# Kernel optimization log

Hardware: AMD Instinct MI355X
Metric: run time of the kernel (lower is better)

Reference implementation:

```python
import jax, jax.numpy as jnp
import numpy as np

B, S, E = 4, 2048, 1024
H, DK = 16, 64

def setup_inputs() -> dict:
    key = jax.random.key(0)
    ks = jax.random.split(key, 9)
    sc = 1.0 / np.sqrt(E)
    return {
        "q": jax.random.normal(ks[0], (B, S, E), jnp.float32),
        "Wq": jax.random.normal(ks[1], (E, H * DK), jnp.float32) * sc,
        "bq": jax.random.normal(ks[2], (H * DK,), jnp.float32) * 0.01,
        "Wk": jax.random.normal(ks[3], (E, H * DK), jnp.float32) * sc,
        "bk": jax.random.normal(ks[4], (H * DK,), jnp.float32) * 0.01,
        "Wv": jax.random.normal(ks[5], (E, H * DK), jnp.float32) * sc,
        "bv": jax.random.normal(ks[6], (H * DK,), jnp.float32) * 0.01,
        "Wo": jax.random.normal(ks[7], (H * DK, E), jnp.float32) * sc,
        "bo": jax.random.normal(ks[8], (E,), jnp.float32) * 0.01,
    }

def _split_heads(x):
    # (B, S, H*DK) -> (B, H, S, DK)
    return x.reshape(B, S, H, DK).transpose(0, 2, 1, 3)

def reference(q, Wq, bq, Wk, bk, Wv, bv, Wo, bo):
    # self-attention: k = v = q (torch module path when k=v=None)
    qh = _split_heads(q @ Wq + bq)
    kh = _split_heads(q @ Wk + bk)
    vh = _split_heads(q @ Wv + bv)
    scale = 1.0 / jnp.sqrt(jnp.asarray(DK, qh.dtype))
    scores = jnp.einsum("bhqd,bhkd->bhqk", qh, kh) * scale  # (B,H,S,S)
    attn = jax.nn.softmax(scores, axis=-1)
    ctx = jnp.einsum("bhqk,bhkd->bhqd", attn, vh)
    ctx = ctx.transpose(0, 2, 1, 3).reshape(B, S, H * DK)
    return ctx @ Wo + bo
```

## Files before the change

kernel.cpp:

```cpp
#include <hip/hip_runtime.h>
#include <hip/hip_bf16.h>
#include <math.h>


typedef _Float16 f16x8 __attribute__((ext_vector_type(8)));
typedef _Float16 f16x4 __attribute__((ext_vector_type(4)));
typedef _Float16 f16x2 __attribute__((ext_vector_type(2)));
typedef float    f32x4 __attribute__((ext_vector_type(4)));
typedef unsigned int u32x2 __attribute__((ext_vector_type(2)));
typedef unsigned int u32x4 __attribute__((ext_vector_type(4)));

#define MFMA16(a,b,c) __builtin_amdgcn_mfma_f32_16x16x32_f16(a,b,c,0,0,0)

__device__ __forceinline__ void async_cp16(const _Float16* g, _Float16* l) {
    __builtin_amdgcn_global_load_lds(
        (const __attribute__((address_space(1))) unsigned int*)g,
        (__attribute__((address_space(3))) unsigned int*)l,
        16, 0, 0);
}

__device__ __forceinline__ f16x2 pk(float a, float b) {
    return __builtin_bit_cast(f16x2, __builtin_amdgcn_cvt_pkrtz(a, b));
}

__global__ void __launch_bounds__(256) prep_weights(
    const float* __restrict__ Wq, const float* __restrict__ Wk,
    const float* __restrict__ Wv, const float* __restrict__ Wo,
    _Float16* __restrict__ wt)
{
    __shared__ float tile[32][33];
    int mat = blockIdx.y;
    const float* W = (mat==0)?Wq:(mat==1)?Wk:(mat==2)?Wv:Wo;
    _Float16* WT = wt + (size_t)mat*1048576;
    int t = blockIdx.x;
    int kb = (t & 31) * 32;
    int nb = (t >> 5) * 32;
    int tx = threadIdx.x & 31, ty = threadIdx.x >> 5;
    #pragma unroll
    for (int r = 0; r < 4; ++r) {
        int row = ty + r*8;
        tile[row][tx] = W[(size_t)(kb+row)*1024 + nb + tx];
    }
    __syncthreads();
    #pragma unroll
    for (int r = 0; r < 4; ++r) {
        int row = ty + r*8;
        WT[(size_t)(nb+row)*1024 + kb + tx] = (_Float16)tile[tx][row];
    }
}

__global__ void __launch_bounds__(256) cvt_x(
    const float* __restrict__ X, _Float16* __restrict__ Xh)
{
    int i = (blockIdx.x*256 + threadIdx.x)*4;
    f32x4 x = *(const f32x4*)&X[i];
    f16x4 h;
    #pragma unroll
    for (int k=0;k<4;k++) h[k] = (_Float16)x[k];
    *(f16x4*)&Xh[i] = h;
}

__device__ __forceinline__ void stage_tile(
    const _Float16* __restrict__ Ag, const _Float16* __restrict__ Bg, int kb,
    _Float16* sAb, _Float16* sBb, int wave, int lane)
{
    #pragma unroll
    for (int j = 0; j < 4; ++j) {
        int d   = j*512 + wave*64 + lane;
        int row = d >> 3;
        int sg  = (d & 7) ^ (row & 7);
        async_cp16(&Ag[(size_t)row*1024 + kb + sg*8], sAb + (j*512 + wave*64)*8);
    }
    #pragma unroll
    for (int j = 0; j < 2; ++j) {
        int d   = j*512 + wave*64 + lane;
        int row = d >> 3;
        int sg  = (d & 7) ^ (row & 7);
        async_cp16(&Bg[(size_t)row*1024 + kb + sg*8], sBb + (j*512 + wave*64)*8);
    }
}

#define GEMM_K_LOOP(EXTRA_STAGE_GUARD)                                         \
    stage_tile(Ag, Bg, 0,  pA0, pB0, wave, lane);                              \
    stage_tile(Ag, Bg, 64, pA1, pB1, wave, lane);                              \
    asm volatile("s_waitcnt vmcnt(6)" ::: "memory");                           \
    __builtin_amdgcn_s_barrier();                                              \
    __builtin_amdgcn_sched_barrier(0);                                         \
    for (int t = 0; t < 16; ++t) {                                             \
        if (t + 2 < 16) stage_tile(Ag, Bg, (t+2)*64, pA2, pB2, wave, lane);    \
        f16x8 af[4][2], bf[4][2];                                              \
        _Pragma("unroll")                                                      \
        for (int i = 0; i < 4; ++i) {                                          \
            _Pragma("unroll")                                                  \
            for (int ks = 0; ks < 2; ++ks) {                                   \
                af[i][ks] = *(const f16x8*)&pA0[(wr*64+i*16+cc)*64 +           \
                                                (((ks*4+q4)^(cc&7))*8)];       \
                bf[i][ks] = *(const f16x8*)&pB0[(wc*64+i*16+cc)*64 +           \
                                                (((ks*4+q4)^(cc&7))*8)];       \
            }                                                                  \
        }                                                                      \
        __builtin_amdgcn_s_setprio(1);                                         \
        _Pragma("unroll")                                                      \
        for (int ks = 0; ks < 2; ++ks)                                         \
            _Pragma("unroll")                                                  \
            for (int i = 0; i < 4; ++i)                                        \
                _Pragma("unroll")                                              \
                for (int j = 0; j < 4; ++j)                                    \
                    acc[i][j] = MFMA16(af[i][ks], bf[j][ks], acc[i][j]);       \
        __builtin_amdgcn_s_setprio(0);                                         \
        if (t < 14) asm volatile("s_waitcnt vmcnt(6)" ::: "memory");           \
        else        asm volatile("s_waitcnt vmcnt(0)" ::: "memory");           \
        __builtin_amdgcn_s_barrier();                                          \
        __builtin_amdgcn_sched_barrier(0);                                     \
        _Float16* tA = pA0; pA0 = pA1; pA1 = pA2; pA2 = tA;                    \
        _Float16* tB = pB0; pB0 = pB1; pB1 = pB2; pB2 = tB;                    \
    }

__global__ void __launch_bounds__(512) gemm_qkv(
    const _Float16* __restrict__ Xh, const _Float16* __restrict__ wt,
    const float* __restrict__ bq, const float* __restrict__ bk, const float* __restrict__ bv,
    _Float16* __restrict__ Q, _Float16* __restrict__ K, _Float16* __restrict__ Vt)
{
    __shared__ __align__(16) _Float16 sA[3][16384];
    __shared__ __align__(16) _Float16 sB[3][8192];

    const int id = blockIdx.x;
    const int msub = id & 7;
    const int t2 = id >> 3;
    const int nblk = t2 % 24;
    const int mblk = (t2 / 24) * 8 + msub;

    const int tid = threadIdx.x;
    const int wave = tid >> 6, lane = tid & 63;
    const int wr = wave >> 1, wc = wave & 1;
    const int q4 = lane >> 4, cc = lane & 15;

    const int mat = nblk >> 3;
    const int colbase = (nblk & 7) * 128;
    const _Float16* Bg = wt + (size_t)mat*1048576 + (size_t)colbase*1024;
    const _Float16* Ag = Xh + (size_t)mblk*262144;

    _Float16 *pA0 = &sA[0][0], *pA1 = &sA[1][0], *pA2 = &sA[2][0];
    _Float16 *pB0 = &sB[0][0], *pB1 = &sB[1][0], *pB2 = &sB[2][0];

    f32x4 acc[4][4] = {};

    GEMM_K_LOOP()

    const float* bias = (mat==0)?bq:(mat==1)?bk:bv;
    const float QSCALE = 0.125f * 1.44269504f;
    #pragma unroll
    for (int i=0;i<4;i++)
      #pragma unroll
      for (int j=0;j<4;j++)
        #pragma unroll
        for (int r=0;r<4;r++){
            int m = mblk*256 + wr*64 + i*16 + q4*4 + r;
            int ncol = colbase + wc*64 + j*16 + cc;
            float val = acc[i][j][r] + bias[ncol];
            int b = m >> 11, s = m & 2047;
            int h = ncol >> 6, dk = ncol & 63;
            if (mat == 2) {
                Vt[((size_t)(b*16+h)*64 + dk)*2048 + s] = (_Float16)val;
            } else {
                size_t qi = ((size_t)(b*16+h)*2048 + s)*64 + dk;
                if (mat == 0) Q[qi] = (_Float16)(val * QSCALE);
                else          K[qi] = (_Float16)val;
            }
        }
}

__global__ void __launch_bounds__(512) gemm_out(
    const _Float16* __restrict__ Ctx, const _Float16* __restrict__ wt,
    const float* __restrict__ bo,
    float* __restrict__ out)
{
    __shared__ __align__(16) _Float16 sA[3][16384];
    __shared__ __align__(16) _Float16 sB[3][8192];

    const int id = blockIdx.x;
    const int msub = id & 7;
    const int t2 = id >> 3;
    const int nblk = t2 & 7;
    const int mblk = (t2 >> 3) * 8 + msub;

    const int tid = threadIdx.x;
    const int wave = tid >> 6, lane = tid & 63;
    const int wr = wave >> 1, wc = wave & 1;
    const int q4 = lane >> 4, cc = lane & 15;

    const _Float16* Bg = wt + (size_t)3*1048576 + (size_t)nblk*128*1024;
    const _Float16* Ag = Ctx + (size_t)mblk*262144;

    _Float16 *pA0 = &sA[0][0], *pA1 = &sA[1][0], *pA2 = &sA[2][0];
    _Float16 *pB0 = &sB[0][0], *pB1 = &sB[1][0], *pB2 = &sB[2][0];

    f32x4 acc[4][4] = {};

    GEMM_K_LOOP()

    #pragma unroll
    for (int i=0;i<4;i++)
      #pragma unroll
      for (int j=0;j<4;j++)
        #pragma unroll
        for (int r=0;r<4;r++){
            int m = mblk*256 + wr*64 + i*16 + q4*4 + r;
            int n = nblk*128 + wc*64 + j*16 + cc;
            out[(size_t)m*1024 + n] = acc[i][j][r] + bo[n];
        }
}

__global__ void __launch_bounds__(256,3) attn(
    const _Float16* __restrict__ Qg, const _Float16* __restrict__ Kg,
    const _Float16* __restrict__ Vg,
    _Float16* __restrict__ Ctx)
{
    __shared__ __align__(16) _Float16 sK[128][72];
    __shared__ __align__(16) _Float16 sV[64][136];

    const int id = blockIdx.x;
    const int xcd = id & 7;
    const int t2 = id >> 3;
    const int qc = t2 & 15;
    const int bh = (t2 >> 4) * 8 + xcd;

    const int tid = threadIdx.x;
    const int wave = tid >> 6, lane = tid & 63;
    const int q4 = lane >> 4, cc = lane & 15;

    const size_t hoff = (size_t)bh * 131072;
    const _Float16* Qp = Qg + hoff;
    const _Float16* Kp = Kg + hoff;
    const _Float16* Vp = Vg + hoff;

    const int qbase = qc*128 + wave*32;

    f16x8 qf[2][2];
    #pragma unroll
    for (int m=0;m<2;m++)
      #pragma unroll
      for (int ks=0;ks<2;ks++)
        qf[m][ks] = *(const f16x8*)&Qp[(qbase+m*16+cc)*64 + ks*32 + q4*8];

    f32x4 o[2][4] = {};
    float lsum[2] = {0.f, 0.f};

    const int r0 = tid >> 3, c8 = (tid & 7)*8;
    const int vrow = tid >> 4, vg = (tid & 15)*8;

    f16x8 kr[4], vr[4];
    #pragma unroll
    for (int p=0;p<4;p++){
        kr[p] = *(const f16x8*)&Kp[(p*32 + r0)*64 + c8];
        vr[p] = *(const f16x8*)&Vp[(size_t)(p*16 + vrow)*2048 + vg];
    }

    for (int kt = 0; kt < 16; ++kt) {
        __syncthreads();
        #pragma unroll
        for (int p=0;p<4;p++){
            *(f16x8*)&sK[p*32+r0][c8] = kr[p];
            *(f16x8*)&sV[p*16+vrow][vg] = vr[p];
        }
        __syncthreads();
        if (kt < 15) {
            #pragma unroll
            for (int p=0;p<4;p++){
                kr[p] = *(const f16x8*)&Kp[((kt+1)*128 + p*32 + r0)*64 + c8];
                vr[p] = *(const f16x8*)&Vp[(size_t)(p*16 + vrow)*2048 + (kt+1)*128 + vg];
            }
        }

        #pragma unroll
        for (int ks=0;ks<4;ks++){
            unsigned Ud[2][2], Wd[2][2];
            #pragma unroll
            for (int aa=0;aa<2;aa++){
                int kj = ks*2 + aa;
                f16x8 k0 = *(const f16x8*)&sK[kj*16+cc][q4*8];
                f16x8 k1 = *(const f16x8*)&sK[kj*16+cc][32+q4*8];
                #pragma unroll
                for (int m=0;m<2;m++){
                    f32x4 z = {};
                    f32x4 s = MFMA16(k0, qf[m][0], z);
                    s = MFMA16(k1, qf[m][1], s);
                    float p0 = __builtin_amdgcn_exp2f(s[0]);
                    float p1 = __builtin_amdgcn_exp2f(s[1]);
                    float p2 = __builtin_amdgcn_exp2f(s[2]);
                    float p3 = __builtin_amdgcn_exp2f(s[3]);
                    lsum[m] += (p0 + p1) + (p2 + p3);
                    unsigned d0 = __builtin_bit_cast(unsigned, pk(p0, p1));
                    unsigned d1 = __builtin_bit_cast(unsigned, pk(p2, p3));
                    if (aa == 0) { Ud[m][0] = d0; Ud[m][1] = d1; }
                    else         { Wd[m][0] = d0; Wd[m][1] = d1; }
                }
            }
            f16x8 pa[2];
            #pragma unroll
            for (int m=0;m<2;m++){
                u32x2 x0 = __builtin_amdgcn_permlane32_swap(Ud[m][0], Wd[m][0], false, false);
                u32x2 r02 = __builtin_amdgcn_permlane16_swap(x0[0], x0[1], false, false);
                u32x2 x1 = __builtin_amdgcn_permlane32_swap(Ud[m][1], Wd[m][1], false, false);
                u32x2 r13 = __builtin_amdgcn_permlane16_swap(x1[0], x1[1], false, false);
                u32x4 pw;
                pw[0] = r02[0]; pw[1] = r13[0]; pw[2] = r02[1]; pw[3] = r13[1];
                pa[m] = __builtin_bit_cast(f16x8, pw);
            }
            #pragma unroll
            for (int v=0;v<4;v++){
                f16x8 vf = *(const f16x8*)&sV[v*16+cc][ks*32+q4*8];
                o[0][v] = MFMA16(pa[0], vf, o[0][v]);
                o[1][v] = MFMA16(pa[1], vf, o[1][v]);
            }
        }
    }

    #pragma unroll
    for (int m=0;m<2;m++){
        lsum[m] += __shfl_xor(lsum[m], 16, 64);
        lsum[m] += __shfl_xor(lsum[m], 32, 64);
    }
    __syncthreads();
    float* sL = (float*)&sK[0][0];
    if (q4 == 0) {
        sL[wave*32 + cc]      = lsum[0];
        sL[wave*32 + 16 + cc] = lsum[1];
    }
    __syncthreads();

    int b = bh >> 4, h = bh & 15;
    #pragma unroll
    for (int m=0;m<2;m++)
      #pragma unroll
      for (int r=0;r<4;r++){
        float inv = 1.f / sL[wave*32 + m*16 + q4*4 + r];
        int s = qbase + m*16 + q4*4 + r;
        #pragma unroll
        for (int v=0;v<4;v++){
            float val = o[m][v][r]*inv;
            int dk = v*16 + cc;
            Ctx[((size_t)(b*2048+s)*16 + h)*64 + dk] = (_Float16)val;
        }
      }
}

extern "C" void kernel_launch(void* const* d_in, const int* in_sizes, int n_in,
                              void* d_out, int out_size, void* d_ws, size_t ws_size,
                              hipStream_t stream)
{
    const float* q  = (const float*)d_in[0];
    const float* Wq = (const float*)d_in[1];
    const float* bq = (const float*)d_in[2];
    const float* Wk = (const float*)d_in[3];
    const float* bk = (const float*)d_in[4];
    const float* Wv = (const float*)d_in[5];
    const float* bv = (const float*)d_in[6];
    const float* Wo = (const float*)d_in[7];
    const float* bo = (const float*)d_in[8];
    float* out = (float*)d_out;

    _Float16* ws  = (_Float16*)d_ws;
    _Float16* wt  = ws;
    _Float16* Xh  = ws + 4194304;
    _Float16* Q   = ws + 12582912;
    _Float16* K   = ws + 20971520;
    _Float16* Vt  = ws + 29360128;
    _Float16* Ctx = Xh;

    prep_weights<<<dim3(1024,4), 256, 0, stream>>>(Wq, Wk, Wv, Wo, wt);
    cvt_x<<<dim3(8192), 256, 0, stream>>>(q, Xh);
    gemm_qkv<<<dim3(768), 512, 0, stream>>>(Xh, wt, bq, bk, bv, Q, K, Vt);
    attn<<<dim3(1024), 256, 0, stream>>>(Q, K, Vt, Ctx);
    gemm_out<<<dim3(256), 512, 0, stream>>>(Ctx, wt, bo, out);
}
```

Baseline: 303.8 us.

## Transpose GEMM tiles to 128x256 and split K-step into two interleaved half-phases

Both projection GEMMs switch from a 256x128 tile to a 128x256 tile, with the wave grid transposed (2 rows by 4 columns of waves) and the block index mapping adjusted. Each 64-wide K step is split into two 32-wide halves. Before each half's MFMAs, the LDS fragments are loaded and half of the next-next tile's global-to-LDS copies are issued, with extra barriers between the halves. The aim is to spread async copy issue across the MFMA phases and cut register pressure from fragment arrays. The cost is more barriers per iteration. The vmcnt(6) wait count still has to match the 3 and 3 split of loads.

After: 303.8 us. About the same (+0.0%).

```diff
diff --git a/kernel.cpp b/kernel.cpp
--- a/kernel.cpp
+++ b/kernel.cpp
@@ -60,19 +60,29 @@
     *(f16x4*)&Xh[i] = h;
 }
 
-__device__ __forceinline__ void stage_tile(
+__device__ __forceinline__ void stage3a(
     const _Float16* __restrict__ Ag, const _Float16* __restrict__ Bg, int kb,
     _Float16* sAb, _Float16* sBb, int wave, int lane)
 {
     #pragma unroll
-    for (int j = 0; j < 4; ++j) {
+    for (int j = 0; j < 2; ++j) {
         int d   = j*512 + wave*64 + lane;
         int row = d >> 3;
         int sg  = (d & 7) ^ (row & 7);
         async_cp16(&Ag[(size_t)row*1024 + kb + sg*8], sAb + (j*512 + wave*64)*8);
     }
-    #pragma unroll
-    for (int j = 0; j < 2; ++j) {
+    {
+        int d   = wave*64 + lane;
+        int row = d >> 3;
+        int sg  = (d & 7) ^ (row & 7);
+        async_cp16(&Bg[(size_t)row*1024 + kb + sg*8], sBb + (wave*64)*8);
+    }
+}
+__device__ __forceinline__ void stage3b(
+    const _Float16* __restrict__ Bg, int kb, _Float16* sBb, int wave, int lane)
+{
+    #pragma unroll
+    for (int j = 1; j < 4; ++j) {
         int d   = j*512 + wave*64 + lane;
         int row = d >> 3;
         int sg  = (d & 7) ^ (row & 7);
@@ -80,38 +90,65 @@
     }
 }
 
-#define GEMM_K_LOOP(EXTRA_STAGE_GUARD)                                         \
-    stage_tile(Ag, Bg, 0,  pA0, pB0, wave, lane);                              \
-    stage_tile(Ag, Bg, 64, pA1, pB1, wave, lane);                              \
+#define GEMM_PIPE_LOOP()                                                       \
+    stage3a(Ag, Bg, 0,  pA0, pB0, wave, lane);                                 \
+    stage3b(Bg, 0,  pB0, wave, lane);                                          \
+    stage3a(Ag, Bg, 64, pA1, pB1, wave, lane);                                 \
+    stage3b(Bg, 64, pB1, wave, lane);                                          \
     asm volatile("s_waitcnt vmcnt(6)" ::: "memory");                           \
     __builtin_amdgcn_s_barrier();                                              \
     __builtin_amdgcn_sched_barrier(0);                                         \
     for (int t = 0; t < 16; ++t) {                                             \
-        if (t + 2 < 16) stage_tile(Ag, Bg, (t+2)*64, pA2, pB2, wave, lane);    \
-        f16x8 af[4][2], bf[4][2];                                              \
-        _Pragma("unroll")                                                      \
-        for (int i = 0; i < 4; ++i) {                                          \
+                    \
+        f16x8 af0[4], bf0[4];                                                  \
+        _Pragma("unroll")                                                      \
+        for (int i = 0; i < 4; ++i)                                            \
+            af0[i] = *(const f16x8*)&pA0[(wr*64+i*16+cc)*64 +                  \
+                                         ((q4^(cc&7))*8)];                     \
+        _Pragma("unroll")                                                      \
+        for (int j = 0; j < 4; ++j)                                            \
+            bf0[j] = *(const f16x8*)&pB0[(wc*64+j*16+cc)*64 +                  \
+                                         ((q4^(cc&7))*8)];                     \
+        if (t < 14) stage3a(Ag, Bg, (t+2)*64, pA2, pB2, wave, lane);           \
+        __builtin_amdgcn_sched_barrier(0);                                     \
+        __builtin_amdgcn_s_barrier();                                          \
+        asm volatile("s_waitcnt lgkmcnt(0)" ::: "memory");                     \
+        __builtin_amdgcn_sched_barrier(0);                                     \
+        __builtin_amdgcn_s_setprio(1);                                         \
+        _Pragma("unroll")                                                      \
+        for (int i = 0; i < 4; ++i)                                            \
             _Pragma("unroll")                                                  \
-            for (int ks = 0; ks < 2; ++ks) {                                   \
-                af[i][ks] = *(const f16x8*)&pA0[(wr*64+i*16+cc)*64 +           \
-                                                (((ks*4+q4)^(cc&7))*8)];       \
-                bf[i][ks] = *(const f16x8*)&pB0[(wc*64+i*16+cc)*64 +           \
-                                                (((ks*4+q4)^(cc&7))*8)];       \
-            }                                                                  \
-        }                                                                      \
+            for (int j = 0; j < 4; ++j)                                        \
+                acc[i][j] = MFMA16(af0[i], bf0[j], acc[i][j]);                 \
+        __builtin_amdgcn_s_setprio(0);                                         \
+        __builtin_amdgcn_sched_barrier(0);                                     \
+        __builtin_amdgcn_s_barrier();                                          \
+            \
+        f16x8 af1[4], bf1[4];                                                  \
+        _Pragma("unroll")                                                      \
+        for (int i = 0; i < 4; ++i)                                            \
+            af1[i] = *(const f16x8*)&pA0[(wr*64+i*16+cc)*64 +                  \
+                                         (((4+q4)^(cc&7))*8)];                 \
+        _Pragma("unroll")                                                      \
+        for (int j = 0; j < 4; ++j)                                            \
+            bf1[j] = *(const f16x8*)&pB0[(wc*64+j*16+cc)*64 +                  \
+                                         (((4+q4)^(cc&7))*8)];                 \
+        if (t < 14) stage3b(Bg, (t+2)*64, pB2, wave, lane);                    \
+        __builtin_amdgcn_sched_barrier(0);                                     \
+        __builtin_amdgcn_s_barrier();                                          \
+        asm volatile("s_waitcnt lgkmcnt(0)" ::: "memory");                     \
+        __builtin_amdgcn_sched_barrier(0);                                     \
         __builtin_amdgcn_s_setprio(1);                                         \
         _Pragma("unroll")                                                      \
-        for (int ks = 0; ks < 2; ++ks)                                         \
+        for (int i = 0; i < 4; ++i)                                            \
             _Pragma("unroll")                                                  \
-            for (int i = 0; i < 4; ++i)                                        \
-                _Pragma("unroll")                                              \
-                for (int j = 0; j < 4; ++j)                                    \
-                    acc[i][j] = MFMA16(af[i][ks], bf[j][ks], acc[i][j]);       \
+            for (int j = 0; j < 4; ++j)                                        \
+                acc[i][j] = MFMA16(af1[i], bf1[j], acc[i][j]);                 \
         __builtin_amdgcn_s_setprio(0);                                         \
         if (t < 14) asm volatile("s_waitcnt vmcnt(6)" ::: "memory");           \
         else        asm volatile("s_waitcnt vmcnt(0)" ::: "memory");           \
+        __builtin_amdgcn_sched_barrier(0);                                     \
         __builtin_amdgcn_s_barrier();                                          \
-        __builtin_amdgcn_sched_barrier(0);                                     \
         _Float16* tA = pA0; pA0 = pA1; pA1 = pA2; pA2 = tA;                    \
         _Float16* tB = pB0; pB0 = pB1; pB1 = pB2; pB2 = tB;                    \
     }
@@ -121,31 +158,31 @@
     const float* __restrict__ bq, const float* __restrict__ bk, const float* __restrict__ bv,
     _Float16* __restrict__ Q, _Float16* __restrict__ K, _Float16* __restrict__ Vt)
 {
-    __shared__ __align__(16) _Float16 sA[3][16384];
-    __shared__ __align__(16) _Float16 sB[3][8192];
+    __shared__ __align__(16) _Float16 sA[3][8192];
+    __shared__ __align__(16) _Float16 sB[3][16384];
 
     const int id = blockIdx.x;
     const int msub = id & 7;
     const int t2 = id >> 3;
-    const int nblk = t2 % 24;
-    const int mblk = (t2 / 24) * 8 + msub;
+    const int nblk = t2 % 12;
+    const int mblk = (t2 / 12) * 8 + msub;
 
     const int tid = threadIdx.x;
     const int wave = tid >> 6, lane = tid & 63;
-    const int wr = wave >> 1, wc = wave & 1;
+    const int wr = wave & 1, wc = wave >> 1;
     const int q4 = lane >> 4, cc = lane & 15;
 
-    const int mat = nblk >> 3;
-    const int colbase = (nblk & 7) * 128;
+    const int mat = nblk >> 2;
+    const int colbase = (nblk & 3) * 256;
     const _Float16* Bg = wt + (size_t)mat*1048576 + (size_t)colbase*1024;
-    const _Float16* Ag = Xh + (size_t)mblk*262144;
+    const _Float16* Ag = Xh + (size_t)mblk*131072;
 
     _Float16 *pA0 = &sA[0][0], *pA1 = &sA[1][0], *pA2 = &sA[2][0];
     _Float16 *pB0 = &sB[0][0], *pB1 = &sB[1][0], *pB2 = &sB[2][0];
 
     f32x4 acc[4][4] = {};
 
-    GEMM_K_LOOP()
+    GEMM_PIPE_LOOP()
 
     const float* bias = (mat==0)?bq:(mat==1)?bk:bv;
     const float QSCALE = 0.125f * 1.44269504f;
@@ -155,7 +192,7 @@
       for (int j=0;j<4;j++)
         #pragma unroll
         for (int r=0;r<4;r++){
-            int m = mblk*256 + wr*64 + i*16 + q4*4 + r;
+            int m = mblk*128 + wr*64 + i*16 + q4*4 + r;
             int ncol = colbase + wc*64 + j*16 + cc;
             float val = acc[i][j][r] + bias[ncol];
             int b = m >> 11, s = m & 2047;
@@ -175,29 +212,29 @@
     const float* __restrict__ bo,
     float* __restrict__ out)
 {
-    __shared__ __align__(16) _Float16 sA[3][16384];
-    __shared__ __align__(16) _Float16 sB[3][8192];
+    __shared__ __align__(16) _Float16 sA[3][8192];
+    __shared__ __align__(16) _Float16 sB[3][16384];
 
     const int id = blockIdx.x;
     const int msub = id & 7;
     const int t2 = id >> 3;
-    const int nblk = t2 & 7;
-    const int mblk = (t2 >> 3) * 8 + msub;
+    const int nblk = t2 & 3;
+    const int mblk = (t2 >> 2) * 8 + msub;
 
     const int tid = threadIdx.x;
     const int wave = tid >> 6, lane = tid & 63;
-    const int wr = wave >> 1, wc = wave & 1;
+    const int wr = wave & 1, wc = wave >> 1;
     const int q4 = lane >> 4, cc = lane & 15;
 
-    const _Float16* Bg = wt + (size_t)3*1048576 + (size_t)nblk*128*1024;
-    const _Float16* Ag = Ctx + (size_t)mblk*262144;
+    const _Float16* Bg = wt + (size_t)3*1048576 + (size_t)nblk*256*1024;
+    const _Float16* Ag = Ctx + (size_t)mblk*131072;
 
     _Float16 *pA0 = &sA[0][0], *pA1 = &sA[1][0], *pA2 = &sA[2][0];
     _Float16 *pB0 = &sB[0][0], *pB1 = &sB[1][0], *pB2 = &sB[2][0];
 
     f32x4 acc[4][4] = {};
 
-    GEMM_K_LOOP()
+    GEMM_PIPE_LOOP()
 
     #pragma unroll
     for (int i=0;i<4;i++)
@@ -205,8 +242,8 @@
       for (int j=0;j<4;j++)
         #pragma unroll
         for (int r=0;r<4;r++){
-            int m = mblk*256 + wr*64 + i*16 + q4*4 + r;
-            int n = nblk*128 + wc*64 + j*16 + cc;
+            int m = mblk*128 + wr*64 + i*16 + q4*4 + r;
+            int n = nblk*256 + wc*64 + j*16 + cc;
             out[(size_t)m*1024 + n] = acc[i][j][r] + bo[n];
         }
 }
```
